# Optimization experiments

Measured on AMD Instinct MI355X. Metric: run time of the kernel, lower is better.

## Reference

```python
import jax, jax.numpy as jnp
import numpy as np

CH = 8        # MASK_HEAD.CHANNELS
CIN = 8       # MASK_BRANCH.OUT_CHANNELS
# weight/bias split offsets for 3-layer head with rel coords:
# w0=(CIN+2)*CH=80, w1=CH*CH=64, w2=CH*1=8, b0=8, b1=8, b2=1 -> 169


def _bilinear_align_corners(x, Ho, Wo):
    # x: [n, c, H, W] -> [n, c, Ho, Wo], matches F.interpolate(align_corners=True)
    n, c, H, W = x.shape
    ys = jnp.arange(Ho, dtype=x.dtype) * ((H - 1) / (Ho - 1))
    xs = jnp.arange(Wo, dtype=x.dtype) * ((W - 1) / (Wo - 1))
    y0 = jnp.floor(ys).astype(jnp.int32)
    y1 = jnp.minimum(y0 + 1, H - 1)
    wy = (ys - y0.astype(x.dtype))[:, None]
    x0 = jnp.floor(xs).astype(jnp.int32)
    x1 = jnp.minimum(x0 + 1, W - 1)
    wx = xs - x0.astype(x.dtype)
    rows = x[..., y0, :] * (1.0 - wy) + x[..., y1, :] * wy   # [n,c,Ho,W]
    out = rows[..., x0] * (1.0 - wx) + rows[..., x1] * wx    # [n,c,Ho,Wo]
    return out


def setup_inputs() -> dict:
    key = jax.random.key(0)
    k1, k2, k3, k4, k5, k6 = jax.random.split(key, 6)
    N, H, W = 2, 128, 192
    n_inst = 256
    stride = 8
    mask_feats = jax.random.normal(k1, (N, CIN, H, W), dtype=jnp.float32)
    mask_head_params = jax.random.normal(k2, (n_inst, 169), dtype=jnp.float32) * 0.1
    # instance center locations in image coords (stride-8 feature covers [0, W*stride))
    instance_locations = jax.random.uniform(k3, (n_inst, 2), dtype=jnp.float32) * jnp.array(
        [W * stride, H * stride], dtype=jnp.float32
    )
    fpn_levels = jax.random.randint(k4, (n_inst,), 0, 5, dtype=jnp.int32)
    soi_table = jnp.array([64.0, 128.0, 256.0, 512.0, 1024.0], dtype=jnp.float32)
    sizes_of_interest = soi_table[fpn_levels]  # pre-gathered soi per instance
    im_inds = jax.random.randint(k5, (n_inst,), 0, N, dtype=jnp.int32)
    return {
        "mask_feats": mask_feats,
        "mask_head_params": mask_head_params,
        "instance_locations": instance_locations,
        "sizes_of_interest": sizes_of_interest,
        "im_inds": im_inds,
        "fpn_levels": fpn_levels,
        "mask_feat_stride": 8,
    }


def reference(mask_feats, mask_head_params, instance_locations, sizes_of_interest,
              im_inds, fpn_levels, mask_feat_stride):
    N, _, H, W = mask_feats.shape
    n_inst = mask_head_params.shape[0]
    dt = mask_feats.dtype

    # compute_locations(H, W, stride): (x, y) centers of the mask-feat grid
    shifts_x = jnp.arange(W, dtype=dt) * mask_feat_stride + mask_feat_stride // 2
    shifts_y = jnp.arange(H, dtype=dt) * mask_feat_stride + mask_feat_stride // 2
    xx, yy = jnp.meshgrid(shifts_x, shifts_y)              # [H, W]
    locations = jnp.stack([xx.ravel(), yy.ravel()], axis=1)  # [HW, 2]

    # relative coords per instance, normalized by size-of-interest of its FPN level
    rel = instance_locations[:, None, :] - locations[None, :, :]   # [n, HW, 2]
    rel = jnp.transpose(rel, (0, 2, 1)) / sizes_of_interest[:, None, None]  # [n, 2, HW]

    feats = mask_feats[im_inds].reshape(n_inst, CIN, H * W)        # gather per instance
    x = jnp.concatenate([rel.astype(dt), feats], axis=1).reshape(n_inst, CIN + 2, H, W)

    p = mask_head_params
    w0 = p[:, 0:80].reshape(n_inst, CH, CIN + 2)
    w1 = p[:, 80:144].reshape(n_inst, CH, CH)
    w2 = p[:, 144:152].reshape(n_inst, 1, CH)
    b0 = p[:, 152:160]
    b1 = p[:, 160:168]
    b2 = p[:, 168:169]

    # per-instance 1x1 convs == batched small GEMMs over the spatial grid
    x = jax.nn.relu(jnp.einsum('noc,nchw->nohw', w0, x) + b0[:, :, None, None])
    x = jax.nn.relu(jnp.einsum('noc,nchw->nohw', w1, x) + b1[:, :, None, None])
    x = jnp.einsum('noc,nchw->nohw', w2, x) + b2[:, :, None, None]  # [n,1,H,W]

    # inference path: F.interpolate(scale_factor=2, mode='bilinear', align_corners=True)
    return _bilinear_align_corners(x, 2 * H, 2 * W)
```

## Files before the change

kernel.cpp:

```cpp
#include <hip/hip_runtime.h>

typedef float f32x2 __attribute__((ext_vector_type(2)));
typedef float f32x4 __attribute__((ext_vector_type(4)));

#define HH 128
#define WW 192
#define HO 256
#define WO 384
#define NINST 256
#define OTY 16
#define LTY 10
#define LPAD 196
#define STRIPS 24

static __device__ __forceinline__ f32x2 splat2(float v) { f32x2 r; r.x = v; r.y = v; return r; }

static __device__ __forceinline__ f32x2 pkfma(f32x2 a, float w, f32x2 c) {
#if __has_builtin(__builtin_elementwise_fma)
    return __builtin_elementwise_fma(a, splat2(w), c);
#else
    f32x2 r; r.x = fmaf(a.x, w, c.x); r.y = fmaf(a.y, w, c.y); return r;
#endif
}

static __device__ __forceinline__ f32x2 relu2(f32x2 a) {
#if __has_builtin(__builtin_elementwise_max)
    return __builtin_elementwise_max(a, splat2(0.0f));
#else
    f32x2 r; r.x = fmaxf(a.x, 0.0f); r.y = fmaxf(a.y, 0.0f); return r;
#endif
}

__global__ __launch_bounds__(256) void dynmask_fused(
    const float* __restrict__ feats,
    const float* __restrict__ params,
    const float* __restrict__ locs,
    const float* __restrict__ soi,
    const int*   __restrict__ im_inds,
    const int*   __restrict__ stride_p,
    float* __restrict__ out)
{
    const int n   = blockIdx.y;
    const int t   = threadIdx.x;
    const int oy0 = blockIdx.x * OTY;

    __shared__ float tile[LTY][LPAD];

    const float sy = 127.0f / 255.0f;
    const float sx = 191.0f / 383.0f;
    const int ly0 = (int)((float)oy0 * sy);

    const float* __restrict__ pw = params + n * 169;
    const int   stride  = *stride_p;
    const float inv_soi = 1.0f / soi[n];
    const float loc_x   = locs[2*n+0];
    const float loc_y   = locs[2*n+1];
    const float* fbase  = feats + im_inds[n] * (8*HH*WW);
    const float xstep   = -(float)stride * inv_soi;

    if (t < LTY * STRIPS) {
        const int r  = (unsigned)t / STRIPS;
        const int c0 = (t - r*STRIPS) * 8;
        int gy = ly0 + r; if (gy > HH-1) gy = HH-1;
        const float* frow = fbase + gy*WW + c0;

        const float yrel = (loc_y - (float)(gy*stride + (stride>>1))) * inv_soi;
        const float xr0  = (loc_x - (float)(c0*stride + (stride>>1))) * inv_soi;

        #pragma unroll
        for (int g = 0; g < 2; ++g) {
            f32x4 f[8];
            #pragma unroll
            for (int ch = 0; ch < 8; ++ch)
                f[ch] = *(const f32x4*)(frow + ch*(HH*WW) + g*4);

            f32x2 xp0, xp1;
            xp0.x = fmaf((float)(g*4+0), xstep, xr0);
            xp0.y = fmaf((float)(g*4+1), xstep, xr0);
            xp1.x = fmaf((float)(g*4+2), xstep, xr0);
            xp1.y = fmaf((float)(g*4+3), xstep, xr0);

            f32x2 h0a[8], h0b[8];
            #pragma unroll
            for (int o = 0; o < 8; ++o) {
                const float byo = fmaf(yrel, pw[o*10+1], pw[152+o]);
                const float wxw = pw[o*10+0];
                f32x2 a0 = pkfma(xp0, wxw, splat2(byo));
                f32x2 a1 = pkfma(xp1, wxw, splat2(byo));
                #pragma unroll
                for (int ch = 0; ch < 8; ++ch) {
                    const float w = pw[o*10+2+ch];
                    a0 = pkfma(f[ch].xy, w, a0);
                    a1 = pkfma(f[ch].zw, w, a1);
                }
                h0a[o] = relu2(a0);
                h0b[o] = relu2(a1);
            }

            f32x2 res0 = splat2(pw[168]);
            f32x2 res1 = splat2(pw[168]);
            #pragma unroll
            for (int o = 0; o < 8; ++o) {
                const float b1w = pw[160+o];
                const float w2w = pw[144+o];
                f32x2 a0 = splat2(b1w);
                f32x2 a1 = splat2(b1w);
                #pragma unroll
                for (int c = 0; c < 8; ++c) {
                    const float w = pw[80+o*8+c];
                    a0 = pkfma(h0a[c], w, a0);
                    a1 = pkfma(h0b[c], w, a1);
                }
                res0 = pkfma(relu2(a0), w2w, res0);
                res1 = pkfma(relu2(a1), w2w, res1);
            }

            f32x4 rv; rv.x = res0.x; rv.y = res0.y; rv.z = res1.x; rv.w = res1.y;
            *(f32x4*)&tile[r][c0 + g*4] = rv;
        }
    }

    __syncthreads();

    float* obase = out + (size_t)n * (HO*WO);
    #pragma unroll
    for (int k = 0; k < 3; ++k) {
        const int u    = t + k*256;
        const int wrap = (u >= 384);
        const int col  = wrap ? u - 384 : u;
        const int r0o  = wrap ? 8 : 0;

        const float xsf = (float)col * sx;
        int ix0 = (int)xsf; if (ix0 > WW-2) ix0 = WW-2;
        const float wx = xsf - (float)ix0;
        const float* tcol = &tile[0][0] + ix0;

        float a, b, c, d;
        int prevIy = -999;
        float* optr = obase + (size_t)(oy0 + r0o) * WO + col;

        for (int rr = 0; rr < 8; ++rr) {
            const int   yo  = oy0 + r0o + rr;
            const float ysf = (float)yo * sy;
            int iy0 = (int)ysf; if (iy0 > HH-2) iy0 = HH-2;
            const float wy = ysf - (float)iy0;

            if (iy0 != prevIy) {
                const float* p = tcol + (iy0 - ly0) * LPAD;
                if (iy0 == prevIy + 1) {
                    a = c; b = d;
                    c = p[LPAD]; d = p[LPAD+1];
                } else {
                    a = p[0];    b = p[1];
                    c = p[LPAD]; d = p[LPAD+1];
                }
                prevIy = iy0;
            }

            float va = fmaf(wy, c - a, a);
            float vb = fmaf(wy, d - b, b);
            *optr = fmaf(wx, vb - va, va);
            optr += WO;
        }
    }
}

extern "C" void kernel_launch(void* const* d_in, const int* in_sizes, int n_in,
                              void* d_out, int out_size, void* d_ws, size_t ws_size,
                              hipStream_t stream) {
    const float* feats    = (const float*)d_in[0];
    const float* params   = (const float*)d_in[1];
    const float* locs     = (const float*)d_in[2];
    const float* soi      = (const float*)d_in[3];
    const int*   im_inds  = (const int*)d_in[4];
    const int*   stride_p = (const int*)d_in[6];
    float* out = (float*)d_out;

    dim3 grid(HO / OTY, NINST);
    dim3 block(256);
    hipLaunchKernelGGL(dynmask_fused, grid, block, 0, stream,
                       feats, params, locs, soi, im_inds, stride_p, out);
}
```

Before: 50.62 us.

## Use fp16 packed dot2 for per-instance MLP with pre-converted half weights

Adds a prep kernel that converts the dynamic head parameters to fp16 in the workspace, with a padded per-instance stride. The main kernel then packs features and hidden activations to half pairs and evaluates the three 1x1 layers with v_dot2 instructions, halving the FMA count. The aim is to cut ALU work in the compute phase. In exchange it adds an extra launch, conversion instructions and fp16 rounding error. If the workspace is too small it falls back to an fp32 scalar path.

New measurement: 54.96 us. 1.09x slower.

```diff
diff --git a/kernel.cpp b/kernel.cpp
--- a/kernel.cpp
+++ b/kernel.cpp
@@ -2,6 +2,7 @@
 
 typedef float f32x2 __attribute__((ext_vector_type(2)));
 typedef float f32x4 __attribute__((ext_vector_type(4)));
+typedef _Float16 h16x2 __attribute__((ext_vector_type(2)));
 
 #define HH 128
 #define WW 192
@@ -12,26 +13,203 @@
 #define LTY 10
 #define LPAD 196
 #define STRIPS 24
-
-static __device__ __forceinline__ f32x2 splat2(float v) { f32x2 r; r.x = v; r.y = v; return r; }
-
-static __device__ __forceinline__ f32x2 pkfma(f32x2 a, float w, f32x2 c) {
-#if __has_builtin(__builtin_elementwise_fma)
-    return __builtin_elementwise_fma(a, splat2(w), c);
+#define PSTRIDE 170
+#define WS_NEED (NINST * PSTRIDE * 2)
+
+static __device__ __forceinline__ unsigned pkrtz(float a, float b) {
+    return __builtin_bit_cast(unsigned, __builtin_amdgcn_cvt_pkrtz(a, b));
+}
+
+static __device__ __forceinline__ float dot2(unsigned a, unsigned b, float c) {
+#if __has_builtin(__builtin_amdgcn_fdot2)
+    return __builtin_amdgcn_fdot2(__builtin_bit_cast(h16x2, a),
+                                  __builtin_bit_cast(h16x2, b), c, false);
 #else
-    f32x2 r; r.x = fmaf(a.x, w, c.x); r.y = fmaf(a.y, w, c.y); return r;
+    h16x2 x = __builtin_bit_cast(h16x2, a), y = __builtin_bit_cast(h16x2, b);
+    return fmaf((float)x[1], (float)y[1], fmaf((float)x[0], (float)y[0], c));
 #endif
 }
 
-static __device__ __forceinline__ f32x2 relu2(f32x2 a) {
-#if __has_builtin(__builtin_elementwise_max)
-    return __builtin_elementwise_max(a, splat2(0.0f));
-#else
-    f32x2 r; r.x = fmaxf(a.x, 0.0f); r.y = fmaxf(a.y, 0.0f); return r;
-#endif
+__global__ __launch_bounds__(256) void prep_params(const float* __restrict__ p,
+                                                   unsigned short* __restrict__ o16) {
+    int j = blockIdx.x * 256 + threadIdx.x;
+    if (j < NINST * 169) {
+        int n = j / 169, k = j - n * 169;
+        _Float16 h = (_Float16)p[j];
+        o16[n * PSTRIDE + k] = __builtin_bit_cast(unsigned short, h);
+    }
 }
 
 __global__ __launch_bounds__(256) void dynmask_fused(
+    const float* __restrict__ feats,
+    const float* __restrict__ params,
+    const unsigned short* __restrict__ params16,
+    const float* __restrict__ locs,
+    const float* __restrict__ soi,
+    const int*   __restrict__ im_inds,
+    const int*   __restrict__ stride_p,
+    float* __restrict__ out)
+{
+    const int n   = blockIdx.y;
+    const int t   = threadIdx.x;
+    const int oy0 = blockIdx.x * OTY;
+
+    __shared__ float tile[LTY][LPAD];
+
+    const float sy = 127.0f / 255.0f;
+    const float sx = 191.0f / 383.0f;
+    const int ly0 = (int)((float)oy0 * sy);
+
+    const float* __restrict__ pw = params + n * 169;
+    const unsigned short* __restrict__ pw16 = params16 + n * PSTRIDE;
+    const int   stride  = *stride_p;
+    const float inv_soi = 1.0f / soi[n];
+    const float loc_x   = locs[2*n+0];
+    const float loc_y   = locs[2*n+1];
+    const float* fbase  = feats + im_inds[n] * (8*HH*WW);
+    const float xstep   = -(float)stride * inv_soi;
+
+    #define W0P(o,kp) (*(const unsigned*)(pw16 + (o)*10 + 2 + 2*(kp)))
+    #define W1P(o,kp) (*(const unsigned*)(pw16 + 80 + (o)*8 + 2*(kp)))
+    #define W2P(kp)   (*(const unsigned*)(pw16 + 144 + 2*(kp)))
+
+    if (t < LTY * STRIPS) {
+        const int r  = (unsigned)t / STRIPS;
+        const int c0 = (t - r*STRIPS) * 8;
+        int gy = ly0 + r; if (gy > HH-1) gy = HH-1;
+        const float* frow = fbase + gy*WW + c0;
+
+        const float yrel = (loc_y - (float)(gy*stride + (stride>>1))) * inv_soi;
+        const float xr0  = (loc_x - (float)(c0*stride + (stride>>1))) * inv_soi;
+
+        float wxw[8], byo[8];
+        #pragma unroll
+        for (int o = 0; o < 8; ++o) {
+            wxw[o] = pw[o*10+0];
+            byo[o] = fmaf(yrel, pw[o*10+1], pw[152+o]);
+        }
+
+        #pragma unroll
+        for (int g = 0; g < 2; ++g) {
+            f32x4 f[8];
+            #pragma unroll
+            for (int ch = 0; ch < 8; ++ch)
+                f[ch] = *(const f32x4*)(frow + ch*(HH*WW) + g*4);
+
+            float xr[4];
+            #pragma unroll
+            for (int j = 0; j < 4; ++j)
+                xr[j] = fmaf((float)(g*4+j), xstep, xr0);
+
+            unsigned fp[4][4];
+            #pragma unroll
+            for (int cp = 0; cp < 4; ++cp)
+                #pragma unroll
+                for (int j = 0; j < 4; ++j)
+                    fp[cp][j] = pkrtz(f[2*cp][j], f[2*cp+1][j]);
+
+            float h0[4][8];
+            #pragma unroll
+            for (int o = 0; o < 8; ++o) {
+                #pragma unroll
+                for (int j = 0; j < 4; ++j) {
+                    float a = fmaf(xr[j], wxw[o], byo[o]);
+                    a = dot2(fp[0][j], W0P(o,0), a);
+                    a = dot2(fp[1][j], W0P(o,1), a);
+                    a = dot2(fp[2][j], W0P(o,2), a);
+                    a = dot2(fp[3][j], W0P(o,3), a);
+                    h0[j][o] = fmaxf(a, 0.0f);
+                }
+            }
+
+            unsigned hp[4][4];
+            #pragma unroll
+            for (int j = 0; j < 4; ++j)
+                #pragma unroll
+                for (int cp = 0; cp < 4; ++cp)
+                    hp[j][cp] = pkrtz(h0[j][2*cp], h0[j][2*cp+1]);
+
+            float h1[4][8];
+            #pragma unroll
+            for (int o = 0; o < 8; ++o) {
+                #pragma unroll
+                for (int j = 0; j < 4; ++j) {
+                    float a = pw[160+o];
+                    a = dot2(hp[j][0], W1P(o,0), a);
+                    a = dot2(hp[j][1], W1P(o,1), a);
+                    a = dot2(hp[j][2], W1P(o,2), a);
+                    a = dot2(hp[j][3], W1P(o,3), a);
+                    h1[j][o] = fmaxf(a, 0.0f);
+                }
+            }
+
+            f32x4 rv;
+            #pragma unroll
+            for (int j = 0; j < 4; ++j) {
+                unsigned p0 = pkrtz(h1[j][0], h1[j][1]);
+                unsigned p1 = pkrtz(h1[j][2], h1[j][3]);
+                unsigned p2 = pkrtz(h1[j][4], h1[j][5]);
+                unsigned p3 = pkrtz(h1[j][6], h1[j][7]);
+                float a = pw[168];
+                a = dot2(p0, W2P(0), a);
+                a = dot2(p1, W2P(1), a);
+                a = dot2(p2, W2P(2), a);
+                a = dot2(p3, W2P(3), a);
+                rv[j] = a;
+            }
+            *(f32x4*)&tile[r][c0 + g*4] = rv;
+        }
+    }
+
+    __syncthreads();
+
+    float* obase = out + (size_t)n * (HO*WO);
+    #pragma unroll
+    for (int k = 0; k < 3; ++k) {
+        const int u    = t + k*256;
+        const int wrap = (u >= 384);
+        const int col  = wrap ? u - 384 : u;
+        const int r0o  = wrap ? 8 : 0;
+
+        const float xsf = (float)col * sx;
+        int ix0 = (int)xsf; if (ix0 > WW-2) ix0 = WW-2;
+        const float wx = xsf - (float)ix0;
+        const float* tcol = &tile[0][0] + ix0;
+
+        float a, b, c, d;
+        int prevIy = -999;
+        float* optr = obase + (size_t)(oy0 + r0o) * WO + col;
+
+        for (int rr = 0; rr < 8; ++rr) {
+            const int   yo  = oy0 + r0o + rr;
+            const float ysf = (float)yo * sy;
+            int iy0 = (int)ysf; if (iy0 > HH-2) iy0 = HH-2;
+            const float wy = ysf - (float)iy0;
+
+            if (iy0 != prevIy) {
+                const float* p = tcol + (iy0 - ly0) * LPAD;
+                if (iy0 == prevIy + 1) {
+                    a = c; b = d;
+                    c = p[LPAD]; d = p[LPAD+1];
+                } else {
+                    a = p[0];    b = p[1];
+                    c = p[LPAD]; d = p[LPAD+1];
+                }
+                prevIy = iy0;
+            }
+
+            float va = fmaf(wy, c - a, a);
+            float vb = fmaf(wy, d - b, b);
+            *optr = fmaf(wx, vb - va, va);
+            optr += WO;
+        }
+    }
+    #undef W0P
+    #undef W1P
+    #undef W2P
+}
+
+__global__ __launch_bounds__(256) void dynmask_fused_f32(
     const float* __restrict__ feats,
     const float* __restrict__ params,
     const float* __restrict__ locs,
@@ -74,48 +252,42 @@
             for (int ch = 0; ch < 8; ++ch)
                 f[ch] = *(const f32x4*)(frow + ch*(HH*WW) + g*4);
 
-            f32x2 xp0, xp1;
-            xp0.x = fmaf((float)(g*4+0), xstep, xr0);
-            xp0.y = fmaf((float)(g*4+1), xstep, xr0);
-            xp1.x = fmaf((float)(g*4+2), xstep, xr0);
-            xp1.y = fmaf((float)(g*4+3), xstep, xr0);
-
-            f32x2 h0a[8], h0b[8];
+            float xr[4];
+            #pragma unroll
+            for (int j = 0; j < 4; ++j)
+                xr[j] = fmaf((float)(g*4+j), xstep, xr0);
+
+            float h0[4][8];
             #pragma unroll
             for (int o = 0; o < 8; ++o) {
                 const float byo = fmaf(yrel, pw[o*10+1], pw[152+o]);
                 const float wxw = pw[o*10+0];
-                f32x2 a0 = pkfma(xp0, wxw, splat2(byo));
-                f32x2 a1 = pkfma(xp1, wxw, splat2(byo));
-                #pragma unroll
-                for (int ch = 0; ch < 8; ++ch) {
-                    const float w = pw[o*10+2+ch];
-                    a0 = pkfma(f[ch].xy, w, a0);
-                    a1 = pkfma(f[ch].zw, w, a1);
-                }
-                h0a[o] = relu2(a0);
-                h0b[o] = relu2(a1);
-            }
-
-            f32x2 res0 = splat2(pw[168]);
-            f32x2 res1 = splat2(pw[168]);
+                #pragma unroll
+                for (int j = 0; j < 4; ++j) {
+                    float a = fmaf(xr[j], wxw, byo);
+                    #pragma unroll
+                    for (int ch = 0; ch < 8; ++ch)
+                        a = fmaf(f[ch][j], pw[o*10+2+ch], a);
+                    h0[j][o] = fmaxf(a, 0.0f);
+                }
+            }
+
+            f32x4 rv;
+            #pragma unroll
+            for (int j = 0; j < 4; ++j) rv[j] = pw[168];
             #pragma unroll
             for (int o = 0; o < 8; ++o) {
                 const float b1w = pw[160+o];
                 const float w2w = pw[144+o];
-                f32x2 a0 = splat2(b1w);
-                f32x2 a1 = splat2(b1w);
-                #pragma unroll
-                for (int c = 0; c < 8; ++c) {
-                    const float w = pw[80+o*8+c];
-                    a0 = pkfma(h0a[c], w, a0);
-                    a1 = pkfma(h0b[c], w, a1);
-                }
-                res0 = pkfma(relu2(a0), w2w, res0);
-                res1 = pkfma(relu2(a1), w2w, res1);
-            }
-
-            f32x4 rv; rv.x = res0.x; rv.y = res0.y; rv.z = res1.x; rv.w = res1.y;
+                #pragma unroll
+                for (int j = 0; j < 4; ++j) {
+                    float a = b1w;
+                    #pragma unroll
+                    for (int c = 0; c < 8; ++c)
+                        a = fmaf(h0[j][c], pw[80+o*8+c], a);
+                    rv[j] = fmaf(fmaxf(a, 0.0f), w2w, rv[j]);
+                }
+            }
             *(f32x4*)&tile[r][c0 + g*4] = rv;
         }
     }
@@ -178,6 +350,15 @@
 
     dim3 grid(HO / OTY, NINST);
     dim3 block(256);
-    hipLaunchKernelGGL(dynmask_fused, grid, block, 0, stream,
-                       feats, params, locs, soi, im_inds, stride_p, out);
-}
+
+    if (ws_size >= (size_t)WS_NEED) {
+        unsigned short* params16 = (unsigned short*)d_ws;
+        hipLaunchKernelGGL(prep_params, dim3(170), dim3(256), 0, stream,
+                           params, params16);
+        hipLaunchKernelGGL(dynmask_fused, grid, block, 0, stream,
+                           feats, params, params16, locs, soi, im_inds, stride_p, out);
+    } else {
+        hipLaunchKernelGGL(dynmask_fused_f32, grid, block, 0, stream,
+                           feats, params, locs, soi, im_inds, stride_p, out);
+    }
+}
```
